# Kernel optimization log

Hardware: AMD Instinct MI355X
Metric: run time of the kernel (lower is better)

The kernel has to match this reference:

```python
import jax, jax.numpy as jnp
import numpy as np
import math

DIM = 1536
HEADS = 4
DIM_KEY = 64
DIM_VALUE = 64
NUM_REL_POS_FEATURES = 64
SEQ_LEN = 4096  # must match the hard-coded positional buffer seq_len in the torch module
SCALE = DIM_KEY ** -0.5


def positional_embed(seq_len, feature_size):
    # get_positional_embed: central-mask features + sign-antisymmetric copy
    distances = jnp.arange(-seq_len + 1, seq_len)  # (2n-1,)
    nb = feature_size // 2  # one feature fn, 2 components
    pow_rate = math.exp(math.log(seq_len + 1) / nb)
    center_widths = jnp.power(jnp.float32(pow_rate), jnp.arange(1, nb + 1, dtype=jnp.float32)) - 1.0
    emb = (center_widths[None, :] > jnp.abs(distances)[:, None]).astype(jnp.float32)  # (2n-1, nb)
    sign = jnp.sign(distances).astype(jnp.float32)[:, None]
    return jnp.concatenate([emb, sign * emb], axis=-1)  # (2n-1, feature_size)


def setup_inputs() -> dict:
    key = jax.random.key(0)
    ks = jax.random.split(key, 9)
    b, n, dim, h, dk, dv, F = 1, SEQ_LEN, DIM, HEADS, DIM_KEY, DIM_VALUE, NUM_REL_POS_FEATURES
    s = 0.02
    x = jax.random.normal(ks[0], (b, n, dim), dtype=jnp.float32)
    Wq = jax.random.normal(ks[1], (dim, h * dk), dtype=jnp.float32) * s
    Wk = jax.random.normal(ks[2], (dim, h * dk), dtype=jnp.float32) * s
    Wv = jax.random.normal(ks[3], (dim, h * dv), dtype=jnp.float32) * s
    W_rel_k = jax.random.normal(ks[4], (F, h * dk), dtype=jnp.float32) * s
    Wo = jax.random.normal(ks[5], (h * dv, dim), dtype=jnp.float32) * s  # torch inits zeros; random for a meaningful test
    bo = jnp.zeros((dim,), dtype=jnp.float32)
    rel_content_bias = jax.random.normal(ks[6], (1, h, 1, dk), dtype=jnp.float32)
    rel_pos_bias = jax.random.normal(ks[7], (1, h, 1, dk), dtype=jnp.float32)
    return {"x": x, "Wq": Wq, "Wk": Wk, "Wv": Wv, "W_rel_k": W_rel_k, "Wo": Wo, "bo": bo,
            "rel_content_bias": rel_content_bias, "rel_pos_bias": rel_pos_bias}


def reference(x, Wq, Wk, Wv, W_rel_k, Wo, bo, rel_content_bias, rel_pos_bias):
    b, n, _ = x.shape
    h, dk, dv = HEADS, DIM_KEY, DIM_VALUE
    # projections -> (b, h, n, d)
    q = (x @ Wq).reshape(b, n, h, dk).transpose(0, 2, 1, 3) * SCALE
    k = (x @ Wk).reshape(b, n, h, dk).transpose(0, 2, 1, 3)
    v = (x @ Wv).reshape(b, n, h, dv).transpose(0, 2, 1, 3)
    # content logits with content bias
    content_logits = jnp.einsum('bhid,bhjd->bhij', q + rel_content_bias, k)
    # relative-position keys from fixed positional buffer (pos_dropout p=0 -> identity)
    positions = positional_embed(SEQ_LEN, NUM_REL_POS_FEATURES)  # (2n-1, F)
    rel_k = (positions @ W_rel_k).reshape(2 * n - 1, h, dk).transpose(1, 0, 2)  # (h, 2n-1, dk)
    # rel logits then Transformer-XL strided shift: rel_logits[i, j] = r[i, n-1 + j - i]
    r = jnp.einsum('bhid,hjd->bhij', q + rel_pos_bias, rel_k)  # (b, h, n, 2n-1)
    idx = (n - 1) + jnp.arange(n)[None, :] - jnp.arange(n)[:, None]  # (n, n)
    rel_logits = jnp.take_along_axis(r, jnp.broadcast_to(idx[None, None], (b, h, n, n)), axis=-1)
    attn = jax.nn.softmax(content_logits + rel_logits, axis=-1)  # attn_dropout p=0 -> identity
    out = jnp.einsum('bhij,bhjd->bhid', attn, v)
    out = out.transpose(0, 2, 1, 3).reshape(b, n, h * dv)
    return out @ Wo + bo
```

## Files before the change

kernel.cpp:

```cpp
#include <hip/hip_runtime.h>
#include <hip/hip_bf16.h>

#define N_SEQ 4096
#define DIMM  1536
#define NH    4
#define DK    64
#define HD    256
#define QK_SCALE 0.125f
#define WSZ   393216
#define KSPLIT 8
#define LOG2E 1.44269504f

typedef __bf16 bf16x8 __attribute__((ext_vector_type(8)));
typedef unsigned short u16;
typedef u16   u16x8  __attribute__((ext_vector_type(8)));
typedef u16   u16x4  __attribute__((ext_vector_type(4)));
typedef float f32x4  __attribute__((ext_vector_type(4)));
typedef float f32x16 __attribute__((ext_vector_type(16)));
typedef unsigned int u32x4 __attribute__((ext_vector_type(4)));

__device__ inline float b2f(u16 u){
    union { float f; unsigned int i; } v; v.i = ((unsigned int)u) << 16; return v.f;
}
__device__ inline u16 f2b(float f){
    __bf16 h = (__bf16)f;
    return __builtin_bit_cast(u16, h);
}
__device__ inline bf16x8 ldfrag(const u16* p){
    return __builtin_bit_cast(bf16x8, *(const u16x8*)p);
}
__device__ inline f32x16 zero16(){
    f32x16 v;
    #pragma unroll
    for (int i = 0; i < 16; ++i) v[i] = 0.f;
    return v;
}
#define EXP2(x) exp2f(x)

__global__ __launch_bounds__(256) void convwt_kernel(const float* __restrict__ Wq,
    const float* __restrict__ Wk, const float* __restrict__ Wv, u16* __restrict__ Wt){
    int idx = (blockIdx.x * 256 + threadIdx.x) * 8;
    int s = idx / WSZ, off = idx % WSZ;
    int n = off / DIMM, k = off % DIMM;
    const float* W = (s == 0) ? Wq : (s == 1 ? Wk : Wv);
    u16x8 o;
    #pragma unroll
    for (int e = 0; e < 8; ++e) o[e] = f2b(W[(size_t)(k + e) * HD + n]);
    *(u16x8*)&Wt[idx] = o;
}

__global__ __launch_bounds__(256) void fmtab_kernel(unsigned char* __restrict__ fmt,
    const float* __restrict__ Wrel, u16* __restrict__ WsP, u16* __restrict__ WsM){
    int t = threadIdx.x;
    if (blockIdx.x == 16){
        int h = t >> 6, d = t & 63;
        float a1 = 0.f, a2 = 0.f;
        for (int fm = 31; fm >= 0; --fm){
            a1 += Wrel[(size_t)fm * HD + h * DK + d];
            a2 += Wrel[(size_t)(32 + fm) * HD + h * DK + d];
            WsP[(h * 32 + fm) * 64 + d] = f2b(a1 + a2);
            WsM[(h * 32 + fm) * 64 + d] = f2b(a1 - a2);
        }
        return;
    }
    int d = blockIdx.x * 256 + t;
    float lg = logf((float)(N_SEQ + 1)) * (1.0f / 32.0f);
    float ad = (float)d;
    int fm = 0;
    for (int f = 0; f < 32; ++f){
        float cw = expf(lg * (float)(f + 1)) - 1.0f;
        fm += (cw <= ad) ? 1 : 0;
    }
    fmt[d] = (unsigned char)fm;
}

__global__ __launch_bounds__(256) void qkv_kernel(const float* __restrict__ X,
    const u16* __restrict__ Wt,
    u16* __restrict__ Q, u16* __restrict__ K, u16* __restrict__ Vt){
    __shared__ __align__(16) u16 xs[64 * 72];
    __shared__ __align__(16) u16 bs[64 * 72];
    int s  = blockIdx.x >> 2;
    int n0 = (blockIdx.x & 3) * 64;
    int m0 = blockIdx.y * 64;
    int t = threadIdx.x;
    int w = t >> 6, lane = t & 63, qd = lane >> 4, l15 = lane & 15;
    int r  = t >> 3;
    int cv = (t & 7) * 8;
    f32x4 acc[4] = {{0,0,0,0},{0,0,0,0},{0,0,0,0},{0,0,0,0}};

    f32x4 xa[2], xb[2];
    u16x8 wv[2];
    auto LOAD = [&](int k0){
        #pragma unroll
        for (int rep = 0; rep < 2; ++rep){
            int rr = rep * 32 + r;
            size_t xi = (size_t)(m0 + rr) * DIMM + k0 + cv;
            xa[rep] = *(const f32x4*)(X + xi);
            xb[rep] = *(const f32x4*)(X + xi + 4);
            wv[rep] = *(const u16x8*)&Wt[(size_t)s * WSZ + (size_t)(n0 + rr) * DIMM + k0 + cv];
        }
    };
    auto STORE = [&](){
        #pragma unroll
        for (int rep = 0; rep < 2; ++rep){
            int rr = rep * 32 + r;
            u16x8 xv;
            #pragma unroll
            for (int e = 0; e < 4; ++e){ xv[e] = f2b(xa[rep][e]); xv[4 + e] = f2b(xb[rep][e]); }
            *(u16x8*)&xs[rr * 72 + cv] = xv;
            *(u16x8*)&bs[rr * 72 + cv] = wv[rep];
        }
    };

    LOAD(0);
    for (int k0 = 0; k0 < DIMM; k0 += 64){
        STORE();
        __syncthreads();
        if (k0 + 64 < DIMM) LOAD(k0 + 64);
        bf16x8 a0 = ldfrag(&xs[(w * 16 + l15) * 72 +  0 + qd * 8]);
        bf16x8 a1 = ldfrag(&xs[(w * 16 + l15) * 72 + 32 + qd * 8]);
        #pragma unroll
        for (int nt = 0; nt < 4; ++nt){
            bf16x8 b0 = ldfrag(&bs[(nt * 16 + l15) * 72 +  0 + qd * 8]);
            bf16x8 b1 = ldfrag(&bs[(nt * 16 + l15) * 72 + 32 + qd * 8]);
            acc[nt] = __builtin_amdgcn_mfma_f32_16x16x32_bf16(a0, b0, acc[nt], 0, 0, 0);
            acc[nt] = __builtin_amdgcn_mfma_f32_16x16x32_bf16(a1, b1, acc[nt], 0, 0, 0);
        }
        __syncthreads();
    }

    int row0 = m0 + w * 16 + qd * 4;
    if (s == 0){
        #pragma unroll
        for (int nt = 0; nt < 4; ++nt){
            int col = n0 + nt * 16 + l15;
            #pragma unroll
            for (int reg = 0; reg < 4; ++reg)
                Q[(size_t)(row0 + reg) * HD + col] = f2b(acc[nt][reg] * QK_SCALE);
        }
    } else if (s == 1){
        #pragma unroll
        for (int nt = 0; nt < 4; ++nt){
            int col = n0 + nt * 16 + l15;
            #pragma unroll
            for (int reg = 0; reg < 4; ++reg)
                K[(size_t)(row0 + reg) * HD + col] = f2b(acc[nt][reg]);
        }
    } else {
        #pragma unroll
        for (int nt = 0; nt < 4; ++nt){
            int col = n0 + nt * 16 + l15;
            u16x4 pv;
            #pragma unroll
            for (int reg = 0; reg < 4; ++reg) pv[reg] = f2b(acc[nt][reg]);
            *(u16x4*)&Vt[(size_t)col * N_SEQ + row0] = pv;
        }
    }
}

__global__ __launch_bounds__(256) void attn_kernel(const u16* __restrict__ Q,
    const u16* __restrict__ Kg, const u16* __restrict__ Vt,
    const u16* __restrict__ WsPg, const u16* __restrict__ WsMg,
    const unsigned char* __restrict__ fmtg,
    const float* __restrict__ CB, const float* __restrict__ PB,
    u16* __restrict__ OpU, float* __restrict__ mpart, float* __restrict__ lpart){
    __shared__ __align__(16) unsigned char smem[39936];
    u16* Ks   = (u16*)(smem);
    u16* Vts  = (u16*)(smem + 9216);
    u16* Qs   = (u16*)(smem);
    u16* relP = (u16*)(smem + 18432);
    u16* relM = (u16*)(smem + 27136);
    unsigned char* fmt = smem + 35840;
    u16* WsPs = (u16*)(smem + 18432);
    u16* WsMs = (u16*)(smem + 23040);

    int i0   = blockIdx.x * 128;
    int h    = blockIdx.y;
    int half = blockIdx.z;
    int bid  = blockIdx.x * NH + h;
    int jbase = half * (N_SEQ / KSPLIT);
    const int NT = (N_SEQ / KSPLIT) / 64;
    int t = threadIdx.x;
    int w = t >> 6, lane = t & 63, l31 = lane & 31, hbit = lane >> 5;
    int h8 = hbit * 8;
    int i_loc = w * 32 + l31;

    int sr = t >> 3, scv = (t & 7) * 8;
    u16x8 kr0, kr1, vr0, vr1;
    auto LOAD = [&](int j0){
        kr0 = *(const u16x8*)&Kg[(size_t)(j0 + sr)      * HD + h * DK + scv];
        kr1 = *(const u16x8*)&Kg[(size_t)(j0 + 32 + sr) * HD + h * DK + scv];
        vr0 = *(const u16x8*)&Vt[(size_t)(h * 64 + sr)      * N_SEQ + j0 + scv];
        vr1 = *(const u16x8*)&Vt[(size_t)(h * 64 + 32 + sr) * N_SEQ + j0 + scv];
    };
    auto STORE = [&](){
        *(u16x8*)&Ks [(sr)      * 72 + scv] = kr0;
        *(u16x8*)&Ks [(32 + sr) * 72 + scv] = kr1;
        *(u16x8*)&Vts[(sr)      * 72 + scv] = vr0;
        *(u16x8*)&Vts[(32 + sr) * 72 + scv] = vr1;
    };
    LOAD(jbase);

    #pragma unroll
    for (int rep = 0; rep < 4; ++rep){
        int vid = rep * 256 + t;
        int r  = vid >> 3;
        int cv = (vid & 7) * 8;
        *(u16x8*)&Qs[r * 72 + cv] = *(const u16x8*)&Q[(size_t)(i0 + r) * HD + h * DK + cv];
    }
    {
        int r = t >> 3, cv = (t & 7) * 8;
        *(u16x8*)&WsPs[r * 72 + cv] = *(const u16x8*)&WsPg[(h * 32 + r) * 64 + cv];
        *(u16x8*)&WsMs[r * 72 + cv] = *(const u16x8*)&WsMg[(h * 32 + r) * 64 + cv];
    }
    ((uint4*)fmt)[t] = ((const uint4*)fmtg)[t];
    __syncthreads();

    bf16x8 qcF[4], qpF[4];
    #pragma unroll
    for (int kc = 0; kc < 4; ++kc){
        bf16x8 raw = ldfrag(&Qs[i_loc * 72 + kc * 16 + h8]);
        const float* cbp = CB + h * DK + kc * 16 + h8;
        const float* pbp = PB + h * DK + kc * 16 + h8;
        bf16x8 qc, qp;
        #pragma unroll
        for (int e = 0; e < 8; ++e){
            float qf = (float)raw[e];
            qc[e] = (__bf16)((qf + cbp[e]) * LOG2E);
            qp[e] = (__bf16)((qf + pbp[e]) * LOG2E);
        }
        qcF[kc] = qc; qpF[kc] = qp;
    }

    f32x16 rP = zero16(), rM = zero16();
    #pragma unroll
    for (int kc = 0; kc < 4; ++kc){
        bf16x8 aP = ldfrag(&WsPs[l31 * 72 + kc * 16 + h8]);
        bf16x8 aM = ldfrag(&WsMs[l31 * 72 + kc * 16 + h8]);
        rP = __builtin_amdgcn_mfma_f32_32x32x16_bf16(aP, qpF[kc], rP, 0, 0, 0);
        rM = __builtin_amdgcn_mfma_f32_32x32x16_bf16(aM, qpF[kc], rM, 0, 0, 0);
    }
    __syncthreads();

    #pragma unroll
    for (int r = 0; r < 16; ++r){
        int fm = (r & 3) + 8 * (r >> 2) + 4 * hbit;
        relP[i_loc * 34 + fm] = f2b(rP[r]);
        relM[i_loc * 34 + fm] = f2b(rM[r]);
    }
    if (hbit == 0)
        relP[i_loc * 34 + 0] = f2b((rP[0] + rM[0]) * 0.5f);
    STORE();
    __syncthreads();

    float mrow = -1e30f, lacc = 0.f;
    f32x16 oacc0 = zero16(), oacc1 = zero16();

#define MFMA32(A, B, C) __builtin_amdgcn_mfma_f32_32x32x16_bf16(A, B, C, 0, 0, 0)

#define PACK8(ST, WD) { \
    _Pragma("unroll") \
    for (int q_ = 0; q_ < 8; ++q_){ \
        float pa_ = EXP2(ST[2 * q_]     - bias); \
        float pc_ = EXP2(ST[2 * q_ + 1] - bias); \
        lsum += pa_ + pc_; \
        WD[q_] = (unsigned int)f2b(pa_) | ((unsigned int)f2b(pc_) << 16); \
    } }

#define MKFRAG(DST, WD, ZZ) { \
    unsigned int a0_ = WD[(ZZ) * 4 + 0], a1_ = WD[(ZZ) * 4 + 1]; \
    unsigned int b0_ = WD[(ZZ) * 4 + 2], b1_ = WD[(ZZ) * 4 + 3]; \
    unsigned int sh0_ = (unsigned int)__shfl_xor((int)(hbit ? a0_ : b0_), 32); \
    unsigned int sh1_ = (unsigned int)__shfl_xor((int)(hbit ? a1_ : b1_), 32); \
    u32x4 fw_; \
    fw_[0] = hbit ? sh0_ : a0_; \
    fw_[1] = hbit ? sh1_ : a1_; \
    fw_[2] = hbit ? b0_  : sh0_; \
    fw_[3] = hbit ? b1_  : sh1_; \
    DST = __builtin_bit_cast(bf16x8, fw_); }

#define PVSTEP(PF, COL) { \
    oacc0 = MFMA32(PF, ldfrag(&Vts[(l31)      * 72 + (COL) + h8]), oacc0); \
    oacc1 = MFMA32(PF, ldfrag(&Vts[(32 + l31) * 72 + (COL) + h8]), oacc1); }

    const u16* relP_i = relP + i_loc * 34;
    const u16* relM_i = relM + i_loc * 34;

    for (int kt = 0; kt < NT; ++kt){
        int j0 = jbase + kt * 64;
        if (kt + 1 < NT) LOAD(j0 + 64);

        f32x16 st0 = zero16(), st1 = zero16();
        __builtin_amdgcn_s_setprio(1);
        #pragma unroll
        for (int kc = 0; kc < 4; ++kc){
            bf16x8 k0 = ldfrag(&Ks[(l31)      * 72 + kc * 16 + h8]);
            bf16x8 k1 = ldfrag(&Ks[(32 + l31) * 72 + kc * 16 + h8]);
            st0 = MFMA32(k0, qcF[kc], st0);
            st1 = MFMA32(k1, qcF[kc], st1);
        }
        __builtin_amdgcn_s_setprio(0);

        int D = j0 - i0;
        int Di = D - i_loc;
        float relv = 0.f;
        bool fast = false; int fmU = 0; const u16* tabU = relP_i;
        if (D >= 128){
            int fa = fmt[D - 127], fb = fmt[D + 63];
            fast = (fa == fb); fmU = fa; tabU = relP_i;
        } else if (D <= -64){
            int fa = fmt[-D - 63], fb = fmt[-D + 127];
            fast = (fa == fb); fmU = fa; tabU = relM_i;
        }
        if (fast){
            relv = b2f(tabU[fmU]);
        } else {
            #pragma unroll
            for (int r = 0; r < 16; ++r){
                const int jb = (r & 3) + 8 * (r >> 2);
                int jbh = jb + 4 * hbit;
                {
                    int dd = Di + jbh;
                    int ad = dd < 0 ? -dd : dd;
                    int fm = fmt[ad];
                    const u16* tab = (dd >= 0) ? relP_i : relM_i;
                    st0[r] += b2f(tab[fm]);
                }
                {
                    int dd = Di + 32 + jbh;
                    int ad = dd < 0 ? -dd : dd;
                    int fm = fmt[ad];
                    const u16* tab = (dd >= 0) ? relP_i : relM_i;
                    st1[r] += b2f(tab[fm]);
                }
            }
        }

        float mx = st0[0];
        #pragma unroll
        for (int r = 1; r < 16; ++r) mx = fmaxf(mx, st0[r]);
        #pragma unroll
        for (int r = 0; r < 16; ++r) mx = fmaxf(mx, st1[r]);
        mx = fmaxf(mx, __shfl_xor(mx, 32)) + relv;

        if (!__all(mx - mrow <= 11.0f)){
            float mnew = fmaxf(mrow, mx);
            float alpha = EXP2(mrow - mnew);
            mrow = mnew;
            lacc *= alpha;
            #pragma unroll
            for (int r = 0; r < 16; ++r){
                float ar = __shfl(alpha, (r & 3) + 8 * (r >> 2) + 4 * hbit);
                oacc0[r] *= ar; oacc1[r] *= ar;
            }
        }

        float bias = mrow - relv;
        float lsum = 0.f;
        unsigned int wds0[8], wds1[8];
        PACK8(st0, wds0)
        PACK8(st1, wds1)
        lacc += lsum + __shfl_xor(lsum, 32);

        bf16x8 pf0, pf1, pf2, pf3;
        MKFRAG(pf0, wds0, 0)
        MKFRAG(pf1, wds0, 1)
        MKFRAG(pf2, wds1, 0)
        MKFRAG(pf3, wds1, 1)
        __builtin_amdgcn_s_setprio(1);
        PVSTEP(pf0,  0)
        PVSTEP(pf1, 16)
        PVSTEP(pf2, 32)
        PVSTEP(pf3, 48)
        __builtin_amdgcn_s_setprio(0);

        __syncthreads();
        if (kt + 1 < NT) STORE();
        __syncthreads();
    }

    size_t pb = ((size_t)half * 128 + bid) * 128;
    #pragma unroll
    for (int r = 0; r < 16; ++r){
        int iO = w * 32 + (r & 3) + 8 * (r >> 2) + 4 * hbit;
        OpU[(pb + iO) * 64 + l31]      = f2b(oacc0[r]);
        OpU[(pb + iO) * 64 + 32 + l31] = f2b(oacc1[r]);
    }
    if (hbit == 0){
        mpart[pb + i_loc] = mrow;
        lpart[pb + i_loc] = lacc;
    }
#undef MFMA32
#undef PACK8
#undef MKFRAG
#undef PVSTEP
}

__global__ __launch_bounds__(256) void combine_kernel(const u16* __restrict__ OpU,
    const float* __restrict__ mpart, const float* __restrict__ lpart,
    u16* __restrict__ Oatt){
    int i0 = blockIdx.x * 128;
    int h  = blockIdx.y;
    int bid = blockIdx.x * NH + h;
    int t = threadIdx.x;
    int r = t >> 1, cb = (t & 1) * 32;
    size_t pr[8];
    float ms[8], ls[8];
    float m = -1e30f;
    #pragma unroll
    for (int s = 0; s < 8; ++s){
        pr[s] = ((size_t)s * 128 + bid) * 128 + r;
        ms[s] = mpart[pr[s]];
        ls[s] = lpart[pr[s]];
        m = fmaxf(m, ms[s]);
    }
    float den = 0.f, wgt[8];
    #pragma unroll
    for (int s = 0; s < 8; ++s){ wgt[s] = EXP2(ms[s] - m); den += wgt[s] * ls[s]; }
    float inv = 1.0f / fmaxf(den, 1e-30f);
    float o[32];
    #pragma unroll
    for (int e = 0; e < 32; ++e) o[e] = 0.f;
    #pragma unroll
    for (int s = 0; s < 8; ++s){
        #pragma unroll
        for (int c = 0; c < 4; ++c){
            u16x8 a = *(const u16x8*)&OpU[pr[s] * 64 + cb + c * 8];
            #pragma unroll
            for (int e = 0; e < 8; ++e) o[c * 8 + e] += wgt[s] * b2f(a[e]);
        }
    }
    size_t ob = (size_t)(i0 + r) * HD + h * DK + cb;
    #pragma unroll
    for (int c = 0; c < 4; ++c){
        u16x8 rv;
        #pragma unroll
        for (int e = 0; e < 8; ++e) rv[e] = f2b(o[c * 8 + e] * inv);
        *(u16x8*)&Oatt[ob + c * 8] = rv;
    }
}

__global__ __launch_bounds__(256) void oproj_kernel(const u16* __restrict__ A,
    const float* __restrict__ Wo, const float* __restrict__ bo,
    float* __restrict__ out, int m_base){
    __shared__ __align__(16) u16 xs[64 * 72];
    __shared__ __align__(16) u16 bs[64 * 72];
    int m0 = m_base + blockIdx.y * 64;
    int n0 = blockIdx.x * 64;
    int t = threadIdx.x;
    int w = t >> 6, lane = t & 63, qd = lane >> 4, l15 = lane & 15;
    f32x4 acc[4] = {{0,0,0,0},{0,0,0,0},{0,0,0,0},{0,0,0,0}};
    for (int k0 = 0; k0 < HD; k0 += 64){
        #pragma unroll
        for (int rep = 0; rep < 2; ++rep){
            int vid = rep * 256 + t;
            int r  = vid >> 3;
            int cv = (vid & 7) * 8;
            *(u16x8*)&xs[r * 72 + cv] = *(const u16x8*)&A[(size_t)(m0 + r) * HD + k0 + cv];
            size_t wi = (size_t)(k0 + r) * DIMM + n0 + cv;
            f32x4 wa = *(const f32x4*)(Wo + wi), wb = *(const f32x4*)(Wo + wi + 4);
            u16x8 wv;
            #pragma unroll
            for (int e = 0; e < 4; ++e){ wv[e] = f2b(wa[e]); wv[4 + e] = f2b(wb[e]); }
            #pragma unroll
            for (int e = 0; e < 8; ++e) bs[(cv + e) * 72 + r] = wv[e];
        }
        __syncthreads();
        bf16x8 a0 = ldfrag(&xs[(w * 16 + l15) * 72 +  0 + qd * 8]);
        bf16x8 a1 = ldfrag(&xs[(w * 16 + l15) * 72 + 32 + qd * 8]);
        #pragma unroll
        for (int nt = 0; nt < 4; ++nt){
            bf16x8 b0 = ldfrag(&bs[(nt * 16 + l15) * 72 +  0 + qd * 8]);
            bf16x8 b1 = ldfrag(&bs[(nt * 16 + l15) * 72 + 32 + qd * 8]);
            acc[nt] = __builtin_amdgcn_mfma_f32_16x16x32_bf16(a0, b0, acc[nt], 0, 0, 0);
            acc[nt] = __builtin_amdgcn_mfma_f32_16x16x32_bf16(a1, b1, acc[nt], 0, 0, 0);
        }
        __syncthreads();
    }
    #pragma unroll
    for (int nt = 0; nt < 4; ++nt)
        #pragma unroll
        for (int reg = 0; reg < 4; ++reg){
            int row = m0 + w * 16 + qd * 4 + reg;
            int col = n0 + nt * 16 + l15;
            out[(size_t)row * DIMM + col] = acc[nt][reg] + bo[col];
        }
}

extern "C" void kernel_launch(void* const* d_in, const int* in_sizes, int n_in,
                              void* d_out, int out_size, void* d_ws, size_t ws_size,
                              hipStream_t stream){
    const float* X  = (const float*)d_in[0];
    const float* Wq = (const float*)d_in[1];
    const float* Wk = (const float*)d_in[2];
    const float* Wv = (const float*)d_in[3];
    const float* Wr = (const float*)d_in[4];
    const float* Wo = (const float*)d_in[5];
    const float* bo = (const float*)d_in[6];
    const float* CB = (const float*)d_in[7];
    const float* PB = (const float*)d_in[8];
    float* out = (float*)d_out;
    u16* base = (u16*)d_out;

    u16* Qb   = base;
    u16* Kb   = base + 1048576;
    u16* Vt   = base + 2097152;
    u16* Wt   = base + 3145728;
    u16* OpU  = base + 3145728;
    float* mpart = out + 5767168;
    float* lpart = out + 5898240;
    u16* Oatt = base;

    unsigned char* fmtg = (unsigned char*)d_ws;
    u16* WsP = (u16*)((char*)d_ws + 4096);
    u16* WsM = (u16*)((char*)d_ws + 20480);

    convwt_kernel<<<dim3(576), 256, 0, stream>>>(Wq, Wk, Wv, Wt);
    fmtab_kernel<<<dim3(17), 256, 0, stream>>>(fmtg, Wr, WsP, WsM);
    qkv_kernel<<<dim3(12, 64), 256, 0, stream>>>(X, Wt, Qb, Kb, Vt);
    attn_kernel<<<dim3(32, NH, KSPLIT), 256, 0, stream>>>(Qb, Kb, Vt, WsP, WsM,
                                                          fmtg, CB, PB,
                                                          OpU, mpart, lpart);
    combine_kernel<<<dim3(32, NH), 256, 0, stream>>>(OpU, mpart, lpart, Oatt);

    oproj_kernel<<<dim3(24, 58), 256, 0, stream>>>(Oatt, Wo, bo, out, 384);
    oproj_kernel<<<dim3(24,  5), 256, 0, stream>>>(Oatt, Wo, bo, out, 64);
    oproj_kernel<<<dim3(24,  1), 256, 0, stream>>>(Oatt, Wo, bo, out, 0);
}
```

Before: 229.6 us.

## Tile weight transpose through LDS and widen small auxiliary kernels

The weight conversion kernel now transposes 64x64 tiles through padded shared memory, so reads from global memory are coalesced instead of strided gathers. The fmtab prefix-sum block preloads all weight rows into registers before the serial accumulation. The combine kernel is spread over four times as many blocks, with each thread handling 8 columns instead of 32, to raise parallelism and memory-level concurrency. These are small prelude and epilogue kernels, so any saving is bounded by their share of the total time.

```diff
diff --git a/kernel.cpp b/kernel.cpp
--- a/kernel.cpp
+++ b/kernel.cpp
@@ -39,14 +39,34 @@
 
 __global__ __launch_bounds__(256) void convwt_kernel(const float* __restrict__ Wq,
     const float* __restrict__ Wk, const float* __restrict__ Wv, u16* __restrict__ Wt){
-    int idx = (blockIdx.x * 256 + threadIdx.x) * 8;
-    int s = idx / WSZ, off = idx % WSZ;
-    int n = off / DIMM, k = off % DIMM;
+    __shared__ float T[64 * 65];
+    int bid = blockIdx.x;
+    int s = bid / 96, tile = bid % 96;
+    int n0 = (tile / 24) * 64;
+    int k0 = (tile % 24) * 64;
     const float* W = (s == 0) ? Wq : (s == 1 ? Wk : Wv);
-    u16x8 o;
-    #pragma unroll
-    for (int e = 0; e < 8; ++e) o[e] = f2b(W[(size_t)(k + e) * HD + n]);
-    *(u16x8*)&Wt[idx] = o;
+    int t = threadIdx.x;
+    int rA = t >> 3, c8 = (t & 7) * 8;
+    #pragma unroll
+    for (int rep = 0; rep < 2; ++rep){
+        int rr = rep * 32 + rA;
+        const float* p = W + (size_t)(k0 + rr) * HD + n0 + c8;
+        f32x4 a = *(const f32x4*)p, b = *(const f32x4*)(p + 4);
+        #pragma unroll
+        for (int e = 0; e < 4; ++e){
+            T[rr * 65 + c8 + e]     = a[e];
+            T[rr * 65 + c8 + 4 + e] = b[e];
+        }
+    }
+    __syncthreads();
+    #pragma unroll
+    for (int rep = 0; rep < 2; ++rep){
+        int rn = rep * 32 + rA;
+        u16x8 o;
+        #pragma unroll
+        for (int e = 0; e < 8; ++e) o[e] = f2b(T[(c8 + e) * 65 + rn]);
+        *(u16x8*)&Wt[(size_t)s * WSZ + (size_t)(n0 + rn) * DIMM + k0 + c8] = o;
+    }
 }
 
 __global__ __launch_bounds__(256) void fmtab_kernel(unsigned char* __restrict__ fmt,
@@ -54,10 +74,17 @@
     int t = threadIdx.x;
     if (blockIdx.x == 16){
         int h = t >> 6, d = t & 63;
+        float w1[32], w2[32];
+        #pragma unroll
+        for (int fm = 0; fm < 32; ++fm){
+            w1[fm] = Wrel[(size_t)fm * HD + h * DK + d];
+            w2[fm] = Wrel[(size_t)(32 + fm) * HD + h * DK + d];
+        }
         float a1 = 0.f, a2 = 0.f;
+        #pragma unroll
         for (int fm = 31; fm >= 0; --fm){
-            a1 += Wrel[(size_t)fm * HD + h * DK + d];
-            a2 += Wrel[(size_t)(32 + fm) * HD + h * DK + d];
+            a1 += w1[fm];
+            a2 += w2[fm];
             WsP[(h * 32 + fm) * 64 + d] = f2b(a1 + a2);
             WsM[(h * 32 + fm) * 64 + d] = f2b(a1 - a2);
         }
@@ -399,17 +426,18 @@
 __global__ __launch_bounds__(256) void combine_kernel(const u16* __restrict__ OpU,
     const float* __restrict__ mpart, const float* __restrict__ lpart,
     u16* __restrict__ Oatt){
-    int i0 = blockIdx.x * 128;
-    int h  = blockIdx.y;
-    int bid = blockIdx.x * NH + h;
+    int h = blockIdx.y;
     int t = threadIdx.x;
-    int r = t >> 1, cb = (t & 1) * 32;
+    int r = t >> 3, cb = (t & 7) * 8;
+    int i = blockIdx.x * 32 + r;
+    int bid = (i >> 7) * NH + h;
+    int ri = i & 127;
     size_t pr[8];
     float ms[8], ls[8];
     float m = -1e30f;
     #pragma unroll
     for (int s = 0; s < 8; ++s){
-        pr[s] = ((size_t)s * 128 + bid) * 128 + r;
+        pr[s] = ((size_t)s * 128 + bid) * 128 + ri;
         ms[s] = mpart[pr[s]];
         ls[s] = lpart[pr[s]];
         m = fmaxf(m, ms[s]);
@@ -418,26 +446,19 @@
     #pragma unroll
     for (int s = 0; s < 8; ++s){ wgt[s] = EXP2(ms[s] - m); den += wgt[s] * ls[s]; }
     float inv = 1.0f / fmaxf(den, 1e-30f);
-    float o[32];
-    #pragma unroll
-    for (int e = 0; e < 32; ++e) o[e] = 0.f;
+    float o[8];
+    #pragma unroll
+    for (int e = 0; e < 8; ++e) o[e] = 0.f;
     #pragma unroll
     for (int s = 0; s < 8; ++s){
-        #pragma unroll
-        for (int c = 0; c < 4; ++c){
-            u16x8 a = *(const u16x8*)&OpU[pr[s] * 64 + cb + c * 8];
-            #pragma unroll
-            for (int e = 0; e < 8; ++e) o[c * 8 + e] += wgt[s] * b2f(a[e]);
-        }
-    }
-    size_t ob = (size_t)(i0 + r) * HD + h * DK + cb;
-    #pragma unroll
-    for (int c = 0; c < 4; ++c){
-        u16x8 rv;
-        #pragma unroll
-        for (int e = 0; e < 8; ++e) rv[e] = f2b(o[c * 8 + e] * inv);
-        *(u16x8*)&Oatt[ob + c * 8] = rv;
-    }
+        u16x8 a = *(const u16x8*)&OpU[pr[s] * 64 + cb];
+        #pragma unroll
+        for (int e = 0; e < 8; ++e) o[e] += wgt[s] * b2f(a[e]);
+    }
+    u16x8 rv;
+    #pragma unroll
+    for (int e = 0; e < 8; ++e) rv[e] = f2b(o[e] * inv);
+    *(u16x8*)&Oatt[(size_t)i * HD + h * DK + cb] = rv;
 }
 
 __global__ __launch_bounds__(256) void oproj_kernel(const u16* __restrict__ A,
@@ -515,13 +536,13 @@
     u16* WsP = (u16*)((char*)d_ws + 4096);
     u16* WsM = (u16*)((char*)d_ws + 20480);
 
-    convwt_kernel<<<dim3(576), 256, 0, stream>>>(Wq, Wk, Wv, Wt);
+    convwt_kernel<<<dim3(288), 256, 0, stream>>>(Wq, Wk, Wv, Wt);
     fmtab_kernel<<<dim3(17), 256, 0, stream>>>(fmtg, Wr, WsP, WsM);
     qkv_kernel<<<dim3(12, 64), 256, 0, stream>>>(X, Wt, Qb, Kb, Vt);
     attn_kernel<<<dim3(32, NH, KSPLIT), 256, 0, stream>>>(Qb, Kb, Vt, WsP, WsM,
                                                           fmtg, CB, PB,
                                                           OpU, mpart, lpart);
-    combine_kernel<<<dim3(32, NH), 256, 0, stream>>>(OpU, mpart, lpart, Oatt);
+    combine_kernel<<<dim3(128, NH), 256, 0, stream>>>(OpU, mpart, lpart, Oatt);
 
     oproj_kernel<<<dim3(24, 58), 256, 0, stream>>>(Oatt, Wo, bo, out, 384);
     oproj_kernel<<<dim3(24,  5), 256, 0, stream>>>(Oatt, Wo, bo, out, 64);
```

Measured after the change: 223.3 us. -2.8%, faster.
